# Optimization experiments

Hardware: AMD Instinct MI355X
Metric: run time of the kernel (lower is better)

The kernel has to match this reference:

```python
import jax, jax.numpy as jnp
from jax import lax
import numpy as np

S, B, I, H = 1024, 512, 5, 32
G = 4 * H  # torch LSTM gate dim, order: i, f, g, o


def setup_inputs() -> dict:
    key = jax.random.key(0)
    ks = jax.random.split(key, 19)
    n = lambda k, shape, s=0.1: jax.random.normal(k, shape, jnp.float32) * s
    return {
        "x": jax.random.normal(ks[0], (S, B, I), jnp.float32),
        "Wih0": n(ks[1], (G, I)), "Whh0": n(ks[2], (G, H)), "bih0": n(ks[3], (G,)), "bhh0": n(ks[4], (G,)),
        "Wih1": n(ks[5], (G, H)), "Whh1": n(ks[6], (G, H)), "bih1": n(ks[7], (G,)), "bhh1": n(ks[8], (G,)),
        "Wih2": n(ks[9], (G, H)), "Whh2": n(ks[10], (G, H)), "bih2": n(ks[11], (G,)), "bhh2": n(ks[12], (G,)),
        "w1": n(ks[13], (H, H)), "b1": n(ks[14], (H,)),
        "w2": n(ks[15], (H, H)), "b2": n(ks[16], (H,)),
        "w3": n(ks[17], (1, H)), "b3": n(ks[18], (1,)),
    }


def lstm_layer(x, Wih, Whh, bih, bhh):
    # x: [S, B, in]; precompute input projections for all steps (one big GEMM)
    xp = jnp.einsum("sbi,gi->sbg", x, Wih) + bih + bhh  # [S, B, 4H]
    h0 = jnp.zeros((x.shape[1], H), x.dtype)
    c0 = jnp.zeros((x.shape[1], H), x.dtype)

    def step(carry, xg):
        h, c = carry
        gates = xg + h @ Whh.T  # [B, 4H]
        i, f, g, o = jnp.split(gates, 4, axis=-1)
        c = jax.nn.sigmoid(f) * c + jax.nn.sigmoid(i) * jnp.tanh(g)
        h = jax.nn.sigmoid(o) * jnp.tanh(c)
        return (h, c), h

    _, ys = lax.scan(step, (h0, c0), xp)
    return ys  # [S, B, H]


def reference(x, Wih0, Whh0, bih0, bhh0, Wih1, Whh1, bih1, bhh1,
              Wih2, Whh2, bih2, bhh2, w1, b1, w2, b2, w3, b3):
    h = lstm_layer(x, Wih0, Whh0, bih0, bhh0)
    h = lstm_layer(h, Wih1, Whh1, bih1, bhh1)
    h = lstm_layer(h, Wih2, Whh2, bih2, bhh2)  # [S, B, H]
    s, b, hd = h.shape
    y = h.reshape(s * b, hd)
    y = y @ w1.T + b1
    y = y @ w2.T + b2
    y = y @ w3.T + b3
    y = jax.nn.relu(y)
    return y.reshape(s, b, -1)  # [S, B, 1]
```

## Files before the change

kernel.cpp:

```cpp
#include <hip/hip_runtime.h>
#include <math.h>

#define S_LEN 1024
#define BATCH 512
#define HID   32

__device__ __forceinline__ float fast_rcp(float x) { return __builtin_amdgcn_rcpf(x); }

__device__ __forceinline__ float sigmoid_f(float x) {
    return fast_rcp(1.0f + __expf(-x));
}

__device__ __forceinline__ float tanh_f(float x) {
    float t = __expf(-2.0f * fabsf(x));
    float r = (1.0f - t) * fast_rcp(1.0f + t);
    return copysignf(r, x);
}

__global__ __launch_bounds__(192, 2)
void lstm3_fused(const float* __restrict__ x,
                 const float* __restrict__ Wih0, const float* __restrict__ Whh0,
                 const float* __restrict__ bih0, const float* __restrict__ bhh0,
                 const float* __restrict__ Wih1, const float* __restrict__ Whh1,
                 const float* __restrict__ bih1, const float* __restrict__ bhh1,
                 const float* __restrict__ Wih2, const float* __restrict__ Whh2,
                 const float* __restrict__ bih2, const float* __restrict__ bhh2,
                 float* __restrict__ hseq)
{
    const int b = blockIdx.x;
    const int w = threadIdx.x >> 6;
    const int l = threadIdx.x & 63;
    const int j = l & 31;
    const bool lowHalf = (l < 32);
    const int gA = l;
    const int gB = l + 64;

    __shared__ float ring[2][4][HID];
    for (int i = threadIdx.x; i < 2 * 4 * HID; i += 192)
        (&ring[0][0][0])[i] = 0.0f;

    const float* Wih = (w == 0) ? Wih0 : (w == 1) ? Wih1 : Wih2;
    const float* Whh = (w == 0) ? Whh0 : (w == 1) ? Whh1 : Whh2;
    const float* bih = (w == 0) ? bih0 : (w == 1) ? bih1 : bih2;
    const float* bhh = (w == 0) ? bhh0 : (w == 1) ? bhh1 : bhh2;

    float whhA[HID], whhB[HID];
#pragma unroll
    for (int k = 0; k < HID; ++k) {
        whhA[k] = Whh[gA * HID + k];
        whhB[k] = Whh[gB * HID + k];
    }
    float wihA[HID], wihB[HID];
    if (w == 0) {
#pragma unroll
        for (int k = 0; k < 5; ++k) {
            wihA[k] = Wih[gA * 5 + k];
            wihB[k] = Wih[gB * 5 + k];
        }
    } else {
#pragma unroll
        for (int k = 0; k < HID; ++k) {
            wihA[k] = Wih[gA * HID + k];
            wihB[k] = Wih[gB * HID + k];
        }
    }
    const float biasA = bih[gA] + bhh[gA];
    const float biasB = bih[gB] + bhh[gB];

    float c = 0.0f;

    const float* xb0 = x + (size_t)b * 5;
    float xv0 = 0.f, xv1 = 0.f, xv2 = 0.f, xv3 = 0.f, xv4 = 0.f;
    if (w == 0) {
        xv0 = xb0[0]; xv1 = xb0[1]; xv2 = xb0[2]; xv3 = xb0[3]; xv4 = xb0[4];
    }

    __syncthreads();

    for (int t = 0; t < S_LEN + 2; ++t) {
        const int s = t - w;
        const bool active = (s >= 0) && (s < S_LEN);
        const int p = t & 1;

        float aA0 = biasA, aA1 = 0.f, aA2 = 0.f, aA3 = 0.f;
        float aB0 = biasB, aB1 = 0.f, aB2 = 0.f, aB3 = 0.f;

        const float4* hown4 = reinterpret_cast<const float4*>(&ring[p][w + 1][0]);
#pragma unroll
        for (int k4 = 0; k4 < HID / 4; ++k4) {
            float4 hv = hown4[k4];
            aA0 += whhA[4 * k4 + 0] * hv.x;
            aA1 += whhA[4 * k4 + 1] * hv.y;
            aA2 += whhA[4 * k4 + 2] * hv.z;
            aA3 += whhA[4 * k4 + 3] * hv.w;
            aB0 += whhB[4 * k4 + 0] * hv.x;
            aB1 += whhB[4 * k4 + 1] * hv.y;
            aB2 += whhB[4 * k4 + 2] * hv.z;
            aB3 += whhB[4 * k4 + 3] * hv.w;
        }

        if (w == 0) {
            aA0 += wihA[0] * xv0; aB0 += wihB[0] * xv0;
            aA1 += wihA[1] * xv1; aB1 += wihB[1] * xv1;
            aA2 += wihA[2] * xv2; aB2 += wihB[2] * xv2;
            aA3 += wihA[3] * xv3; aB3 += wihB[3] * xv3;
            aA0 += wihA[4] * xv4; aB0 += wihB[4] * xv4;
            if (s + 1 < S_LEN) {
                const float* xn = xb0 + (size_t)(s + 1) * BATCH * 5;
                xv0 = xn[0]; xv1 = xn[1]; xv2 = xn[2]; xv3 = xn[3]; xv4 = xn[4];
            }
        } else {
            const float4* hin4 = reinterpret_cast<const float4*>(&ring[p][w][0]);
#pragma unroll
            for (int k4 = 0; k4 < HID / 4; ++k4) {
                float4 hv = hin4[k4];
                aA0 += wihA[4 * k4 + 0] * hv.x;
                aA1 += wihA[4 * k4 + 1] * hv.y;
                aA2 += wihA[4 * k4 + 2] * hv.z;
                aA3 += wihA[4 * k4 + 3] * hv.w;
                aB0 += wihB[4 * k4 + 0] * hv.x;
                aB1 += wihB[4 * k4 + 1] * hv.y;
                aB2 += wihB[4 * k4 + 2] * hv.z;
                aB3 += wihB[4 * k4 + 3] * hv.w;
            }
        }
        float accA = (aA0 + aA1) + (aA2 + aA3);
        float accB = (aB0 + aB1) + (aB2 + aB3);

        float pA = __shfl_xor(accA, 32);
        float pB = __shfl_xor(accB, 32);
        float gi = lowHalf ? accA : pA;
        float gf = lowHalf ? pA : accA;
        float gg = lowHalf ? accB : pB;
        float go = lowHalf ? pB : accB;

        gi = sigmoid_f(gi);
        gf = sigmoid_f(gf);
        gg = tanh_f(gg);
        go = sigmoid_f(go);
        float c_new = gf * c + gi * gg;
        float h = go * tanh_f(c_new);

        if (active) {
            c = c_new;
            if (lowHalf) {
                ring[p ^ 1][w + 1][j] = h;
                if (w == 2)
                    hseq[((size_t)s * BATCH + b) * HID + j] = h;
            }
        }
        __syncthreads();
    }
}

__global__ __launch_bounds__(256)
void mlp_kernel(const float* __restrict__ h, const float* __restrict__ w1,
                const float* __restrict__ b1, const float* __restrict__ w2,
                const float* __restrict__ b2, const float* __restrict__ w3,
                const float* __restrict__ b3, float* __restrict__ out)
{
    __shared__ float W1[HID * HID];
    __shared__ float W2[HID * HID];
    __shared__ float W3[HID];
    __shared__ float B1[HID];
    __shared__ float B2[HID];
    __shared__ float B3s;

    for (int i = threadIdx.x; i < HID * HID; i += blockDim.x) {
        W1[i] = w1[i];
        W2[i] = w2[i];
    }
    if (threadIdx.x < HID) {
        W3[threadIdx.x] = w3[threadIdx.x];
        B1[threadIdx.x] = b1[threadIdx.x];
        B2[threadIdx.x] = b2[threadIdx.x];
    }
    if (threadIdx.x == 0) B3s = b3[0];
    __syncthreads();

    const size_t e = (size_t)blockIdx.x * blockDim.x + threadIdx.x;
    float hv[HID];
    const float4* hp = reinterpret_cast<const float4*>(h + e * HID);
#pragma unroll
    for (int k4 = 0; k4 < HID / 4; ++k4) {
        float4 v = hp[k4];
        hv[4 * k4 + 0] = v.x;
        hv[4 * k4 + 1] = v.y;
        hv[4 * k4 + 2] = v.z;
        hv[4 * k4 + 3] = v.w;
    }

    float y1[HID];
#pragma unroll
    for (int jj = 0; jj < HID; ++jj) {
        float acc = B1[jj];
#pragma unroll
        for (int k = 0; k < HID; ++k) acc += W1[jj * HID + k] * hv[k];
        y1[jj] = acc;
    }
    float y2[HID];
#pragma unroll
    for (int jj = 0; jj < HID; ++jj) {
        float acc = B2[jj];
#pragma unroll
        for (int k = 0; k < HID; ++k) acc += W2[jj * HID + k] * y1[k];
        y2[jj] = acc;
    }
    float acc3 = B3s;
#pragma unroll
    for (int k = 0; k < HID; ++k) acc3 += W3[k] * y2[k];
    out[e] = fmaxf(acc3, 0.0f);
}

extern "C" void kernel_launch(void* const* d_in, const int* in_sizes, int n_in,
                              void* d_out, int out_size, void* d_ws, size_t ws_size,
                              hipStream_t stream)
{
    const float* x    = (const float*)d_in[0];
    const float* Wih0 = (const float*)d_in[1];
    const float* Whh0 = (const float*)d_in[2];
    const float* bih0 = (const float*)d_in[3];
    const float* bhh0 = (const float*)d_in[4];
    const float* Wih1 = (const float*)d_in[5];
    const float* Whh1 = (const float*)d_in[6];
    const float* bih1 = (const float*)d_in[7];
    const float* bhh1 = (const float*)d_in[8];
    const float* Wih2 = (const float*)d_in[9];
    const float* Whh2 = (const float*)d_in[10];
    const float* bih2 = (const float*)d_in[11];
    const float* bhh2 = (const float*)d_in[12];
    const float* w1   = (const float*)d_in[13];
    const float* b1   = (const float*)d_in[14];
    const float* w2   = (const float*)d_in[15];
    const float* b2   = (const float*)d_in[16];
    const float* w3   = (const float*)d_in[17];
    const float* b3   = (const float*)d_in[18];

    float* hseq = (float*)d_ws;

    lstm3_fused<<<BATCH, 192, 0, stream>>>(x, Wih0, Whh0, bih0, bhh0,
                                           Wih1, Whh1, bih1, bhh1,
                                           Wih2, Whh2, bih2, bhh2, hseq);

    mlp_kernel<<<(S_LEN * BATCH) / 256, 256, 0, stream>>>(hseq, w1, b1, w2, b2, w3, b3,
                                                          (float*)d_out);
}
```

Measured before the change: 942.1 us.

## Split each LSTM layer across two wavefronts with one gate row per lane

Doubles the threads per block to 384, so each layer uses two wavefronts and each lane computes a single gate row instead of two. That halves the per-step dot-product work on the serial critical path. Weights are pre-scaled by log2e, or 2·log2e for the g gate, so every gate goes through one sigmoid via exp2, and tanh(g) is recovered as 2σ(2g)−1. Gates are then gathered with three xor shuffles. The cost is more threads per block, and each __syncthreads now has to synchronise six wavefronts.

```diff
diff --git a/kernel.cpp b/kernel.cpp
--- a/kernel.cpp
+++ b/kernel.cpp
@@ -5,19 +5,12 @@
 #define BATCH 512
 #define HID   32
 
+#define LOG2E 1.44269504088896340736f
+
 __device__ __forceinline__ float fast_rcp(float x) { return __builtin_amdgcn_rcpf(x); }
-
-__device__ __forceinline__ float sigmoid_f(float x) {
-    return fast_rcp(1.0f + __expf(-x));
-}
-
-__device__ __forceinline__ float tanh_f(float x) {
-    float t = __expf(-2.0f * fabsf(x));
-    float r = (1.0f - t) * fast_rcp(1.0f + t);
-    return copysignf(r, x);
-}
-
-__global__ __launch_bounds__(192, 2)
+__device__ __forceinline__ float fast_exp2(float x) { return __builtin_amdgcn_exp2f(x); }
+
+__global__ __launch_bounds__(384, 3)
 void lstm3_fused(const float* __restrict__ x,
                  const float* __restrict__ Wih0, const float* __restrict__ Whh0,
                  const float* __restrict__ bih0, const float* __restrict__ bhh0,
@@ -28,124 +21,134 @@
                  float* __restrict__ hseq)
 {
     const int b = blockIdx.x;
-    const int w = threadIdx.x >> 6;
+    const int w6 = threadIdx.x >> 6;
+    const int layer = w6 >> 1;
+    const int half = w6 & 1;
     const int l = threadIdx.x & 63;
-    const int j = l & 31;
-    const bool lowHalf = (l < 32);
-    const int gA = l;
-    const int gB = l + 64;
+    const int g4 = l >> 4;
+    const int uu = l & 15;
+    const int j = half * 16 + uu;
+    const int tg = g4 ^ (g4 >> 1);
+    const int row = tg * HID + j;
+    const bool sel1 = (g4 & 1) != 0;
+    const bool sel2 = (g4 & 2) != 0;
+    const bool isG = (g4 == 3);
+    const float scale = isG ? (2.0f * LOG2E) : LOG2E;
 
     __shared__ float ring[2][4][HID];
-    for (int i = threadIdx.x; i < 2 * 4 * HID; i += 192)
+    for (int i = threadIdx.x; i < 2 * 4 * HID; i += 384)
         (&ring[0][0][0])[i] = 0.0f;
 
-    const float* Wih = (w == 0) ? Wih0 : (w == 1) ? Wih1 : Wih2;
-    const float* Whh = (w == 0) ? Whh0 : (w == 1) ? Whh1 : Whh2;
-    const float* bih = (w == 0) ? bih0 : (w == 1) ? bih1 : bih2;
-    const float* bhh = (w == 0) ? bhh0 : (w == 1) ? bhh1 : bhh2;
-
-    float whhA[HID], whhB[HID];
-#pragma unroll
-    for (int k = 0; k < HID; ++k) {
-        whhA[k] = Whh[gA * HID + k];
-        whhB[k] = Whh[gB * HID + k];
-    }
-    float wihA[HID], wihB[HID];
-    if (w == 0) {
-#pragma unroll
-        for (int k = 0; k < 5; ++k) {
-            wihA[k] = Wih[gA * 5 + k];
-            wihB[k] = Wih[gB * 5 + k];
-        }
+    const float* Wih = (layer == 0) ? Wih0 : (layer == 1) ? Wih1 : Wih2;
+    const float* Whh = (layer == 0) ? Whh0 : (layer == 1) ? Whh1 : Whh2;
+    const float* bih = (layer == 0) ? bih0 : (layer == 1) ? bih1 : bih2;
+    const float* bhh = (layer == 0) ? bhh0 : (layer == 1) ? bhh1 : bhh2;
+
+    float whh[HID];
+    {
+        const float4* wr = reinterpret_cast<const float4*>(Whh + (size_t)row * HID);
+#pragma unroll
+        for (int k4 = 0; k4 < HID / 4; ++k4) {
+            float4 v = wr[k4];
+            whh[4 * k4 + 0] = v.x * scale;
+            whh[4 * k4 + 1] = v.y * scale;
+            whh[4 * k4 + 2] = v.z * scale;
+            whh[4 * k4 + 3] = v.w * scale;
+        }
+    }
+    float wih[HID];
+    if (layer == 0) {
+#pragma unroll
+        for (int k = 0; k < 5; ++k)
+            wih[k] = Wih[row * 5 + k] * scale;
     } else {
-#pragma unroll
-        for (int k = 0; k < HID; ++k) {
-            wihA[k] = Wih[gA * HID + k];
-            wihB[k] = Wih[gB * HID + k];
-        }
-    }
-    const float biasA = bih[gA] + bhh[gA];
-    const float biasB = bih[gB] + bhh[gB];
+        const float4* wr = reinterpret_cast<const float4*>(Wih + (size_t)row * HID);
+#pragma unroll
+        for (int k4 = 0; k4 < HID / 4; ++k4) {
+            float4 v = wr[k4];
+            wih[4 * k4 + 0] = v.x * scale;
+            wih[4 * k4 + 1] = v.y * scale;
+            wih[4 * k4 + 2] = v.z * scale;
+            wih[4 * k4 + 3] = v.w * scale;
+        }
+    }
+    const float bias = (bih[row] + bhh[row]) * scale;
 
     float c = 0.0f;
 
     const float* xb0 = x + (size_t)b * 5;
     float xv0 = 0.f, xv1 = 0.f, xv2 = 0.f, xv3 = 0.f, xv4 = 0.f;
-    if (w == 0) {
+    if (layer == 0) {
         xv0 = xb0[0]; xv1 = xb0[1]; xv2 = xb0[2]; xv3 = xb0[3]; xv4 = xb0[4];
     }
 
     __syncthreads();
 
     for (int t = 0; t < S_LEN + 2; ++t) {
-        const int s = t - w;
+        const int s = t - layer;
         const bool active = (s >= 0) && (s < S_LEN);
         const int p = t & 1;
 
-        float aA0 = biasA, aA1 = 0.f, aA2 = 0.f, aA3 = 0.f;
-        float aB0 = biasB, aB1 = 0.f, aB2 = 0.f, aB3 = 0.f;
-
-        const float4* hown4 = reinterpret_cast<const float4*>(&ring[p][w + 1][0]);
+        float a0 = bias, a1 = 0.f, a2 = 0.f, a3 = 0.f;
+
+        const float4* hown4 = reinterpret_cast<const float4*>(&ring[p][layer + 1][0]);
 #pragma unroll
         for (int k4 = 0; k4 < HID / 4; ++k4) {
             float4 hv = hown4[k4];
-            aA0 += whhA[4 * k4 + 0] * hv.x;
-            aA1 += whhA[4 * k4 + 1] * hv.y;
-            aA2 += whhA[4 * k4 + 2] * hv.z;
-            aA3 += whhA[4 * k4 + 3] * hv.w;
-            aB0 += whhB[4 * k4 + 0] * hv.x;
-            aB1 += whhB[4 * k4 + 1] * hv.y;
-            aB2 += whhB[4 * k4 + 2] * hv.z;
-            aB3 += whhB[4 * k4 + 3] * hv.w;
-        }
-
-        if (w == 0) {
-            aA0 += wihA[0] * xv0; aB0 += wihB[0] * xv0;
-            aA1 += wihA[1] * xv1; aB1 += wihB[1] * xv1;
-            aA2 += wihA[2] * xv2; aB2 += wihB[2] * xv2;
-            aA3 += wihA[3] * xv3; aB3 += wihB[3] * xv3;
-            aA0 += wihA[4] * xv4; aB0 += wihB[4] * xv4;
+            a0 += whh[4 * k4 + 0] * hv.x;
+            a1 += whh[4 * k4 + 1] * hv.y;
+            a2 += whh[4 * k4 + 2] * hv.z;
+            a3 += whh[4 * k4 + 3] * hv.w;
+        }
+
+        if (layer == 0) {
+            a0 += wih[0] * xv0;
+            a1 += wih[1] * xv1;
+            a2 += wih[2] * xv2;
+            a3 += wih[3] * xv3;
+            a0 += wih[4] * xv4;
             if (s + 1 < S_LEN) {
                 const float* xn = xb0 + (size_t)(s + 1) * BATCH * 5;
                 xv0 = xn[0]; xv1 = xn[1]; xv2 = xn[2]; xv3 = xn[3]; xv4 = xn[4];
             }
         } else {
-            const float4* hin4 = reinterpret_cast<const float4*>(&ring[p][w][0]);
+            const float4* hin4 = reinterpret_cast<const float4*>(&ring[p][layer][0]);
 #pragma unroll
             for (int k4 = 0; k4 < HID / 4; ++k4) {
                 float4 hv = hin4[k4];
-                aA0 += wihA[4 * k4 + 0] * hv.x;
-                aA1 += wihA[4 * k4 + 1] * hv.y;
-                aA2 += wihA[4 * k4 + 2] * hv.z;
-                aA3 += wihA[4 * k4 + 3] * hv.w;
-                aB0 += wihB[4 * k4 + 0] * hv.x;
-                aB1 += wihB[4 * k4 + 1] * hv.y;
-                aB2 += wihB[4 * k4 + 2] * hv.z;
-                aB3 += wihB[4 * k4 + 3] * hv.w;
+                a0 += wih[4 * k4 + 0] * hv.x;
+                a1 += wih[4 * k4 + 1] * hv.y;
+                a2 += wih[4 * k4 + 2] * hv.z;
+                a3 += wih[4 * k4 + 3] * hv.w;
             }
         }
-        float accA = (aA0 + aA1) + (aA2 + aA3);
-        float accB = (aB0 + aB1) + (aB2 + aB3);
-
-        float pA = __shfl_xor(accA, 32);
-        float pB = __shfl_xor(accB, 32);
-        float gi = lowHalf ? accA : pA;
-        float gf = lowHalf ? pA : accA;
-        float gg = lowHalf ? accB : pB;
-        float go = lowHalf ? pB : accB;
-
-        gi = sigmoid_f(gi);
-        gf = sigmoid_f(gf);
-        gg = tanh_f(gg);
-        go = sigmoid_f(go);
-        float c_new = gf * c + gi * gg;
-        float h = go * tanh_f(c_new);
+        const float acc = (a0 + a1) + (a2 + a3);
+
+        const float act = fast_rcp(1.0f + fast_exp2(-acc));
+
+        const float v16 = __shfl_xor(act, 16);
+        const float v32 = __shfl_xor(act, 32);
+        const float v48 = __shfl_xor(v16, 32);
+        const float t0 = sel1 ? v16 : act;
+        const float t1 = sel1 ? act : v16;
+        const float t2 = sel1 ? v48 : v32;
+        const float t3 = sel1 ? v32 : v48;
+        const float ii = sel2 ? t2 : t0;
+        const float ff = sel2 ? t3 : t1;
+        const float oo = sel2 ? t0 : t2;
+        float gg = sel2 ? t1 : t3;
+        gg = 2.0f * gg - 1.0f;
+
+        const float c_new = ff * c + ii * gg;
+        const float e = fast_exp2(-2.0f * LOG2E * fabsf(c_new));
+        const float tc = copysignf((1.0f - e) * fast_rcp(1.0f + e), c_new);
+        const float h = oo * tc;
 
         if (active) {
             c = c_new;
-            if (lowHalf) {
-                ring[p ^ 1][w + 1][j] = h;
-                if (w == 2)
+            if (g4 == 0) {
+                ring[p ^ 1][layer + 1][j] = h;
+                if (layer == 2)
                     hseq[((size_t)s * BATCH + b) * HID + j] = h;
             }
         }
@@ -238,7 +241,7 @@
 
     float* hseq = (float*)d_ws;
 
-    lstm3_fused<<<BATCH, 192, 0, stream>>>(x, Wih0, Whh0, bih0, bhh0,
+    lstm3_fused<<<BATCH, 384, 0, stream>>>(x, Wih0, Whh0, bih0, bhh0,
                                            Wih1, Whh1, bih1, bhh1,
                                            Wih2, Whh2, bih2, bhh2, hseq);
 
```

After: 1.010 ms. +7.2%, slower.

## Run all three LSTM layers in one wavefront with readlane broadcasts

Applied to the files above, without the earlier changes.

Collapses the three-wavefront layer pipeline into a single 64-lane wavefront per batch element that keeps all three layers' weights in registers and wavefront-skews the layers. Hidden state is broadcast with readlane instead of an LDS ring, which removes the per-step __syncthreads and LDS traffic. Weights are pre-scaled by log2e (2·log2e for the g gate) so activations use exp2 directly, and tanh(g) is computed as 2·sigmoid(2g)−1. The cost is about 330 weight registers per lane and three times the serial FMA work per wavefront, which limits occupancy to one wave per block and may cause spills.

```diff
diff --git a/kernel.cpp b/kernel.cpp
--- a/kernel.cpp
+++ b/kernel.cpp
@@ -5,19 +5,51 @@
 #define BATCH 512
 #define HID   32
 
+#define LOG2E 1.44269504088896340736f
+
 __device__ __forceinline__ float fast_rcp(float x) { return __builtin_amdgcn_rcpf(x); }
-
-__device__ __forceinline__ float sigmoid_f(float x) {
-    return fast_rcp(1.0f + __expf(-x));
-}
-
-__device__ __forceinline__ float tanh_f(float x) {
-    float t = __expf(-2.0f * fabsf(x));
-    float r = (1.0f - t) * fast_rcp(1.0f + t);
-    return copysignf(r, x);
-}
-
-__global__ __launch_bounds__(192, 2)
+__device__ __forceinline__ float fast_exp2(float x) { return __builtin_amdgcn_exp2f(x); }
+
+__device__ __forceinline__ float bcast(float v, int k) {
+    return __int_as_float(__builtin_amdgcn_readlane(__float_as_int(v), k));
+}
+
+__device__ __forceinline__ void lstm_tail(float accA, float accB, bool lowHalf,
+                                          float c, float& c_out, float& h_out)
+{
+    float pA = __shfl_xor(accA, 32);
+    float pB = __shfl_xor(accB, 32);
+    float yi = lowHalf ? accA : pA;
+    float yf = lowHalf ? pA : accA;
+    float yg = lowHalf ? accB : pB;
+    float yo = lowHalf ? pB : accB;
+    float gi = fast_rcp(1.0f + fast_exp2(-yi));
+    float gf = fast_rcp(1.0f + fast_exp2(-yf));
+    float sg = fast_rcp(1.0f + fast_exp2(-yg));
+    float go = fast_rcp(1.0f + fast_exp2(-yo));
+    float gg = 2.0f * sg - 1.0f;
+    float cn = gf * c + gi * gg;
+    float e  = fast_exp2(-2.0f * LOG2E * fabsf(cn));
+    float tc = copysignf((1.0f - e) * fast_rcp(1.0f + e), cn);
+    c_out = cn;
+    h_out = go * tc;
+}
+
+#define LOADROW(dst, base, row, sc)                                            \
+    {                                                                          \
+        const float4* W_ = reinterpret_cast<const float4*>((base) +            \
+                                                    (size_t)(row) * HID);      \
+        _Pragma("unroll")                                                      \
+        for (int k4 = 0; k4 < 8; ++k4) {                                       \
+            float4 v_ = W_[k4];                                                \
+            dst[4 * k4 + 0] = v_.x * (sc);                                     \
+            dst[4 * k4 + 1] = v_.y * (sc);                                     \
+            dst[4 * k4 + 2] = v_.z * (sc);                                     \
+            dst[4 * k4 + 3] = v_.w * (sc);                                     \
+        }                                                                      \
+    }
+
+__global__ __launch_bounds__(64)
 void lstm3_fused(const float* __restrict__ x,
                  const float* __restrict__ Wih0, const float* __restrict__ Whh0,
                  const float* __restrict__ bih0, const float* __restrict__ bhh0,
@@ -28,128 +60,81 @@
                  float* __restrict__ hseq)
 {
     const int b = blockIdx.x;
-    const int w = threadIdx.x >> 6;
     const int l = threadIdx.x & 63;
     const int j = l & 31;
     const bool lowHalf = (l < 32);
     const int gA = l;
     const int gB = l + 64;
-
-    __shared__ float ring[2][4][HID];
-    for (int i = threadIdx.x; i < 2 * 4 * HID; i += 192)
-        (&ring[0][0][0])[i] = 0.0f;
-
-    const float* Wih = (w == 0) ? Wih0 : (w == 1) ? Wih1 : Wih2;
-    const float* Whh = (w == 0) ? Whh0 : (w == 1) ? Whh1 : Whh2;
-    const float* bih = (w == 0) ? bih0 : (w == 1) ? bih1 : bih2;
-    const float* bhh = (w == 0) ? bhh0 : (w == 1) ? bhh1 : bhh2;
-
-    float whhA[HID], whhB[HID];
-#pragma unroll
-    for (int k = 0; k < HID; ++k) {
-        whhA[k] = Whh[gA * HID + k];
-        whhB[k] = Whh[gB * HID + k];
-    }
-    float wihA[HID], wihB[HID];
-    if (w == 0) {
-#pragma unroll
-        for (int k = 0; k < 5; ++k) {
-            wihA[k] = Wih[gA * 5 + k];
-            wihB[k] = Wih[gB * 5 + k];
+    const float sA = LOG2E;
+    const float sB = lowHalf ? (2.0f * LOG2E) : LOG2E;
+
+    float whA0[HID], whB0[HID], whA1[HID], whB1[HID], whA2[HID], whB2[HID];
+    float wiA1[HID], wiB1[HID], wiA2[HID], wiB2[HID];
+    float wxA[5], wxB[5];
+
+    LOADROW(whA0, Whh0, gA, sA); LOADROW(whB0, Whh0, gB, sB);
+    LOADROW(whA1, Whh1, gA, sA); LOADROW(whB1, Whh1, gB, sB);
+    LOADROW(whA2, Whh2, gA, sA); LOADROW(whB2, Whh2, gB, sB);
+    LOADROW(wiA1, Wih1, gA, sA); LOADROW(wiB1, Wih1, gB, sB);
+    LOADROW(wiA2, Wih2, gA, sA); LOADROW(wiB2, Wih2, gB, sB);
+#pragma unroll
+    for (int k = 0; k < 5; ++k) {
+        wxA[k] = Wih0[gA * 5 + k] * sA;
+        wxB[k] = Wih0[gB * 5 + k] * sB;
+    }
+    const float b0A = (bih0[gA] + bhh0[gA]) * sA;
+    const float b0B = (bih0[gB] + bhh0[gB]) * sB;
+    const float b1A = (bih1[gA] + bhh1[gA]) * sA;
+    const float b1B = (bih1[gB] + bhh1[gB]) * sB;
+    const float b2A = (bih2[gA] + bhh2[gA]) * sA;
+    const float b2B = (bih2[gB] + bhh2[gB]) * sB;
+
+    float h0d = 0.f, h1d = 0.f, h2d = 0.f;
+    float c0 = 0.f, c1 = 0.f, c2 = 0.f;
+
+    const float* xb = x + (size_t)b * 5;
+    float xv0 = xb[0], xv1 = xb[1], xv2 = xb[2], xv3 = xb[3], xv4 = xb[4];
+
+    for (int t = 0; t < S_LEN + 2; ++t) {
+        float a0A = b0A, a0B = b0B;
+        float a1A = b1A, a1B = b1B;
+        float a2A = b2A, a2B = b2B;
+
+        a0A += wxA[0] * xv0; a0B += wxB[0] * xv0;
+        a0A += wxA[1] * xv1; a0B += wxB[1] * xv1;
+        a0A += wxA[2] * xv2; a0B += wxB[2] * xv2;
+        a0A += wxA[3] * xv3; a0B += wxB[3] * xv3;
+        a0A += wxA[4] * xv4; a0B += wxB[4] * xv4;
+
+#pragma unroll
+        for (int k = 0; k < HID; ++k) {
+            float h0k = bcast(h0d, k);
+            float h1k = bcast(h1d, k);
+            float h2k = bcast(h2d, k);
+            a0A += whA0[k] * h0k; a0B += whB0[k] * h0k;
+            a1A += wiA1[k] * h0k; a1B += wiB1[k] * h0k;
+            a1A += whA1[k] * h1k; a1B += whB1[k] * h1k;
+            a2A += wiA2[k] * h1k; a2B += wiB2[k] * h1k;
+            a2A += whA2[k] * h2k; a2B += whB2[k] * h2k;
         }
-    } else {
-#pragma unroll
-        for (int k = 0; k < HID; ++k) {
-            wihA[k] = Wih[gA * HID + k];
-            wihB[k] = Wih[gB * HID + k];
+
+        float cn, hn;
+        lstm_tail(a2A, a2B, lowHalf, c2, cn, hn);
+        if (t >= 2) {
+            c2 = cn; h2d = hn;
+            if (lowHalf)
+                hseq[((size_t)(t - 2) * BATCH + b) * HID + j] = hn;
         }
-    }
-    const float biasA = bih[gA] + bhh[gA];
-    const float biasB = bih[gB] + bhh[gB];
-
-    float c = 0.0f;
-
-    const float* xb0 = x + (size_t)b * 5;
-    float xv0 = 0.f, xv1 = 0.f, xv2 = 0.f, xv3 = 0.f, xv4 = 0.f;
-    if (w == 0) {
-        xv0 = xb0[0]; xv1 = xb0[1]; xv2 = xb0[2]; xv3 = xb0[3]; xv4 = xb0[4];
-    }
-
-    __syncthreads();
-
-    for (int t = 0; t < S_LEN + 2; ++t) {
-        const int s = t - w;
-        const bool active = (s >= 0) && (s < S_LEN);
-        const int p = t & 1;
-
-        float aA0 = biasA, aA1 = 0.f, aA2 = 0.f, aA3 = 0.f;
-        float aB0 = biasB, aB1 = 0.f, aB2 = 0.f, aB3 = 0.f;
-
-        const float4* hown4 = reinterpret_cast<const float4*>(&ring[p][w + 1][0]);
-#pragma unroll
-        for (int k4 = 0; k4 < HID / 4; ++k4) {
-            float4 hv = hown4[k4];
-            aA0 += whhA[4 * k4 + 0] * hv.x;
-            aA1 += whhA[4 * k4 + 1] * hv.y;
-            aA2 += whhA[4 * k4 + 2] * hv.z;
-            aA3 += whhA[4 * k4 + 3] * hv.w;
-            aB0 += whhB[4 * k4 + 0] * hv.x;
-            aB1 += whhB[4 * k4 + 1] * hv.y;
-            aB2 += whhB[4 * k4 + 2] * hv.z;
-            aB3 += whhB[4 * k4 + 3] * hv.w;
-        }
-
-        if (w == 0) {
-            aA0 += wihA[0] * xv0; aB0 += wihB[0] * xv0;
-            aA1 += wihA[1] * xv1; aB1 += wihB[1] * xv1;
-            aA2 += wihA[2] * xv2; aB2 += wihB[2] * xv2;
-            aA3 += wihA[3] * xv3; aB3 += wihB[3] * xv3;
-            aA0 += wihA[4] * xv4; aB0 += wihB[4] * xv4;
-            if (s + 1 < S_LEN) {
-                const float* xn = xb0 + (size_t)(s + 1) * BATCH * 5;
+        lstm_tail(a1A, a1B, lowHalf, c1, cn, hn);
+        if (t >= 1 && t < S_LEN + 1) { c1 = cn; h1d = hn; }
+        lstm_tail(a0A, a0B, lowHalf, c0, cn, hn);
+        if (t < S_LEN) {
+            c0 = cn; h0d = hn;
+            if (t + 1 < S_LEN) {
+                const float* xn = xb + (size_t)(t + 1) * BATCH * 5;
                 xv0 = xn[0]; xv1 = xn[1]; xv2 = xn[2]; xv3 = xn[3]; xv4 = xn[4];
             }
-        } else {
-            const float4* hin4 = reinterpret_cast<const float4*>(&ring[p][w][0]);
-#pragma unroll
-            for (int k4 = 0; k4 < HID / 4; ++k4) {
-                float4 hv = hin4[k4];
-                aA0 += wihA[4 * k4 + 0] * hv.x;
-                aA1 += wihA[4 * k4 + 1] * hv.y;
-                aA2 += wihA[4 * k4 + 2] * hv.z;
-                aA3 += wihA[4 * k4 + 3] * hv.w;
-                aB0 += wihB[4 * k4 + 0] * hv.x;
-                aB1 += wihB[4 * k4 + 1] * hv.y;
-                aB2 += wihB[4 * k4 + 2] * hv.z;
-                aB3 += wihB[4 * k4 + 3] * hv.w;
-            }
         }
-        float accA = (aA0 + aA1) + (aA2 + aA3);
-        float accB = (aB0 + aB1) + (aB2 + aB3);
-
-        float pA = __shfl_xor(accA, 32);
-        float pB = __shfl_xor(accB, 32);
-        float gi = lowHalf ? accA : pA;
-        float gf = lowHalf ? pA : accA;
-        float gg = lowHalf ? accB : pB;
-        float go = lowHalf ? pB : accB;
-
-        gi = sigmoid_f(gi);
-        gf = sigmoid_f(gf);
-        gg = tanh_f(gg);
-        go = sigmoid_f(go);
-        float c_new = gf * c + gi * gg;
-        float h = go * tanh_f(c_new);
-
-        if (active) {
-            c = c_new;
-            if (lowHalf) {
-                ring[p ^ 1][w + 1][j] = h;
-                if (w == 2)
-                    hseq[((size_t)s * BATCH + b) * HID + j] = h;
-            }
-        }
-        __syncthreads();
     }
 }
 
@@ -238,9 +223,9 @@
 
     float* hseq = (float*)d_ws;
 
-    lstm3_fused<<<BATCH, 192, 0, stream>>>(x, Wih0, Whh0, bih0, bhh0,
-                                           Wih1, Whh1, bih1, bhh1,
-                                           Wih2, Whh2, bih2, bhh2, hseq);
+    lstm3_fused<<<BATCH, 64, 0, stream>>>(x, Wih0, Whh0, bih0, bhh0,
+                                          Wih1, Whh1, bih1, bhh1,
+                                          Wih2, Whh2, bih2, bhh2, hseq);
 
     mlp_kernel<<<(S_LEN * BATCH) / 256, 256, 0, stream>>>(hseq, w1, b1, w2, b2, w3, b3,
                                                           (float*)d_out);
```

New measurement: 1.676 ms. 1.78x slower.

## Prescale LSTM weights by log2e, stage x in LDS, use exp2 and lighter barrier

Applied to the files above, without the earlier changes.

Folds the log2(e) factor, and the factor of 2 for the tanh gate, into the weights and biases at load time. Each gate activation then becomes a raw exp2 plus a reciprocal, and tanh(g) is computed as 2*sigmoid(2g)-1. The whole x sequence for the batch element is staged into shared memory up front, which removes the per-step global load on layer 0's serial path. __syncthreads is replaced by an explicit lgkmcnt wait plus s_barrier that skips waiting on vector memory, so the hseq global stores need not drain each step. The cost is extra LDS use (about 20KB per block), which may affect occupancy, and slightly different rounding.

```diff
diff --git a/kernel.cpp b/kernel.cpp
--- a/kernel.cpp
+++ b/kernel.cpp
@@ -5,17 +5,30 @@
 #define BATCH 512
 #define HID   32
 
+#define LOG2E 1.44269504088896340736f
+
 __device__ __forceinline__ float fast_rcp(float x) { return __builtin_amdgcn_rcpf(x); }
-
-__device__ __forceinline__ float sigmoid_f(float x) {
-    return fast_rcp(1.0f + __expf(-x));
-}
-
-__device__ __forceinline__ float tanh_f(float x) {
-    float t = __expf(-2.0f * fabsf(x));
-    float r = (1.0f - t) * fast_rcp(1.0f + t);
-    return copysignf(r, x);
-}
+__device__ __forceinline__ float fast_exp2(float x) { return __builtin_amdgcn_exp2f(x); }
+
+__device__ __forceinline__ void tick_barrier() {
+    asm volatile("s_waitcnt lgkmcnt(0)" ::: "memory");
+    __builtin_amdgcn_s_barrier();
+    asm volatile("" ::: "memory");
+}
+
+#define LOADROW(dst, base, row, sc)                                            \
+    {                                                                          \
+        const float4* W_ = reinterpret_cast<const float4*>((base) +            \
+                                                    (size_t)(row) * HID);      \
+        _Pragma("unroll")                                                      \
+        for (int k4 = 0; k4 < 8; ++k4) {                                       \
+            float4 v_ = W_[k4];                                                \
+            dst[4 * k4 + 0] = v_.x * (sc);                                     \
+            dst[4 * k4 + 1] = v_.y * (sc);                                     \
+            dst[4 * k4 + 2] = v_.z * (sc);                                     \
+            dst[4 * k4 + 3] = v_.w * (sc);                                     \
+        }                                                                      \
+    }
 
 __global__ __launch_bounds__(192, 2)
 void lstm3_fused(const float* __restrict__ x,
@@ -34,46 +47,50 @@
     const bool lowHalf = (l < 32);
     const int gA = l;
     const int gB = l + 64;
-
+    const float sA = LOG2E;
+    const float sB = lowHalf ? (2.0f * LOG2E) : LOG2E;
+
+    __shared__ float4 xl4[S_LEN];
+    __shared__ float  xl1[S_LEN];
     __shared__ float ring[2][4][HID];
+
     for (int i = threadIdx.x; i < 2 * 4 * HID; i += 192)
         (&ring[0][0][0])[i] = 0.0f;
+    {
+        float* xf = reinterpret_cast<float*>(xl4);
+        for (int idx = threadIdx.x; idx < S_LEN * 5; idx += 192) {
+            const int s = idx / 5;
+            const int c = idx - 5 * s;
+            const float v = x[(size_t)s * (BATCH * 5) + b * 5 + c];
+            if (c < 4) xf[s * 4 + c] = v;
+            else       xl1[s] = v;
+        }
+    }
 
     const float* Wih = (w == 0) ? Wih0 : (w == 1) ? Wih1 : Wih2;
     const float* Whh = (w == 0) ? Whh0 : (w == 1) ? Whh1 : Whh2;
     const float* bih = (w == 0) ? bih0 : (w == 1) ? bih1 : bih2;
     const float* bhh = (w == 0) ? bhh0 : (w == 1) ? bhh1 : bhh2;
 
-    float whhA[HID], whhB[HID];
-#pragma unroll
-    for (int k = 0; k < HID; ++k) {
-        whhA[k] = Whh[gA * HID + k];
-        whhB[k] = Whh[gB * HID + k];
-    }
-    float wihA[HID], wihB[HID];
+    float whA[HID], whB[HID];
+    LOADROW(whA, Whh, gA, sA);
+    LOADROW(whB, Whh, gB, sB);
+    float wiA[HID], wiB[HID];
+    float wxA[5], wxB[5];
     if (w == 0) {
 #pragma unroll
         for (int k = 0; k < 5; ++k) {
-            wihA[k] = Wih[gA * 5 + k];
-            wihB[k] = Wih[gB * 5 + k];
+            wxA[k] = Wih[gA * 5 + k] * sA;
+            wxB[k] = Wih[gB * 5 + k] * sB;
         }
     } else {
-#pragma unroll
-        for (int k = 0; k < HID; ++k) {
-            wihA[k] = Wih[gA * HID + k];
-            wihB[k] = Wih[gB * HID + k];
-        }
-    }
-    const float biasA = bih[gA] + bhh[gA];
-    const float biasB = bih[gB] + bhh[gB];
+        LOADROW(wiA, Wih, gA, sA);
+        LOADROW(wiB, Wih, gB, sB);
+    }
+    const float biasA = (bih[gA] + bhh[gA]) * sA;
+    const float biasB = (bih[gB] + bhh[gB]) * sB;
 
     float c = 0.0f;
-
-    const float* xb0 = x + (size_t)b * 5;
-    float xv0 = 0.f, xv1 = 0.f, xv2 = 0.f, xv3 = 0.f, xv4 = 0.f;
-    if (w == 0) {
-        xv0 = xb0[0]; xv1 = xb0[1]; xv2 = xb0[2]; xv3 = xb0[3]; xv4 = xb0[4];
-    }
 
     __syncthreads();
 
@@ -89,57 +106,61 @@
 #pragma unroll
         for (int k4 = 0; k4 < HID / 4; ++k4) {
             float4 hv = hown4[k4];
-            aA0 += whhA[4 * k4 + 0] * hv.x;
-            aA1 += whhA[4 * k4 + 1] * hv.y;
-            aA2 += whhA[4 * k4 + 2] * hv.z;
-            aA3 += whhA[4 * k4 + 3] * hv.w;
-            aB0 += whhB[4 * k4 + 0] * hv.x;
-            aB1 += whhB[4 * k4 + 1] * hv.y;
-            aB2 += whhB[4 * k4 + 2] * hv.z;
-            aB3 += whhB[4 * k4 + 3] * hv.w;
+            aA0 += whA[4 * k4 + 0] * hv.x;
+            aA1 += whA[4 * k4 + 1] * hv.y;
+            aA2 += whA[4 * k4 + 2] * hv.z;
+            aA3 += whA[4 * k4 + 3] * hv.w;
+            aB0 += whB[4 * k4 + 0] * hv.x;
+            aB1 += whB[4 * k4 + 1] * hv.y;
+            aB2 += whB[4 * k4 + 2] * hv.z;
+            aB3 += whB[4 * k4 + 3] * hv.w;
         }
 
         if (w == 0) {
-            aA0 += wihA[0] * xv0; aB0 += wihB[0] * xv0;
-            aA1 += wihA[1] * xv1; aB1 += wihB[1] * xv1;
-            aA2 += wihA[2] * xv2; aB2 += wihB[2] * xv2;
-            aA3 += wihA[3] * xv3; aB3 += wihB[3] * xv3;
-            aA0 += wihA[4] * xv4; aB0 += wihB[4] * xv4;
-            if (s + 1 < S_LEN) {
-                const float* xn = xb0 + (size_t)(s + 1) * BATCH * 5;
-                xv0 = xn[0]; xv1 = xn[1]; xv2 = xn[2]; xv3 = xn[3]; xv4 = xn[4];
+            if (active) {
+                const float4 xv = xl4[s];
+                const float  x4 = xl1[s];
+                aA0 += wxA[0] * xv.x; aB0 += wxB[0] * xv.x;
+                aA1 += wxA[1] * xv.y; aB1 += wxB[1] * xv.y;
+                aA2 += wxA[2] * xv.z; aB2 += wxB[2] * xv.z;
+                aA3 += wxA[3] * xv.w; aB3 += wxB[3] * xv.w;
+                aA0 += wxA[4] * x4;   aB0 += wxB[4] * x4;
             }
         } else {
             const float4* hin4 = reinterpret_cast<const float4*>(&ring[p][w][0]);
 #pragma unroll
             for (int k4 = 0; k4 < HID / 4; ++k4) {
                 float4 hv = hin4[k4];
-                aA0 += wihA[4 * k4 + 0] * hv.x;
-                aA1 += wihA[4 * k4 + 1] * hv.y;
-                aA2 += wihA[4 * k4 + 2] * hv.z;
-                aA3 += wihA[4 * k4 + 3] * hv.w;
-                aB0 += wihB[4 * k4 + 0] * hv.x;
-                aB1 += wihB[4 * k4 + 1] * hv.y;
-                aB2 += wihB[4 * k4 + 2] * hv.z;
-                aB3 += wihB[4 * k4 + 3] * hv.w;
+                aA0 += wiA[4 * k4 + 0] * hv.x;
+                aA1 += wiA[4 * k4 + 1] * hv.y;
+                aA2 += wiA[4 * k4 + 2] * hv.z;
+                aA3 += wiA[4 * k4 + 3] * hv.w;
+                aB0 += wiB[4 * k4 + 0] * hv.x;
+                aB1 += wiB[4 * k4 + 1] * hv.y;
+                aB2 += wiB[4 * k4 + 2] * hv.z;
+                aB3 += wiB[4 * k4 + 3] * hv.w;
             }
         }
-        float accA = (aA0 + aA1) + (aA2 + aA3);
-        float accB = (aB0 + aB1) + (aB2 + aB3);
-
-        float pA = __shfl_xor(accA, 32);
-        float pB = __shfl_xor(accB, 32);
-        float gi = lowHalf ? accA : pA;
-        float gf = lowHalf ? pA : accA;
-        float gg = lowHalf ? accB : pB;
-        float go = lowHalf ? pB : accB;
-
-        gi = sigmoid_f(gi);
-        gf = sigmoid_f(gf);
-        gg = tanh_f(gg);
-        go = sigmoid_f(go);
-        float c_new = gf * c + gi * gg;
-        float h = go * tanh_f(c_new);
+        const float accA = (aA0 + aA1) + (aA2 + aA3);
+        const float accB = (aB0 + aB1) + (aB2 + aB3);
+
+        const float pA = __shfl_xor(accA, 32);
+        const float pB = __shfl_xor(accB, 32);
+        const float yi = lowHalf ? accA : pA;
+        const float yf = lowHalf ? pA : accA;
+        const float yg = lowHalf ? accB : pB;
+        const float yo = lowHalf ? pB : accB;
+
+        const float gi = fast_rcp(1.0f + fast_exp2(-yi));
+        const float gf = fast_rcp(1.0f + fast_exp2(-yf));
+        const float sg = fast_rcp(1.0f + fast_exp2(-yg));
+        const float go = fast_rcp(1.0f + fast_exp2(-yo));
+        const float gg = 2.0f * sg - 1.0f;
+
+        const float c_new = gf * c + gi * gg;
+        const float e  = fast_exp2(-2.0f * LOG2E * fabsf(c_new));
+        const float tc = copysignf((1.0f - e) * fast_rcp(1.0f + e), c_new);
+        const float h = go * tc;
 
         if (active) {
             c = c_new;
@@ -149,7 +170,7 @@
                     hseq[((size_t)s * BATCH + b) * HID + j] = h;
             }
         }
-        __syncthreads();
+        tick_barrier();
     }
 }
 
```

Result: faster. 908.6 us (-3.6%).
